# Kernel tuning notes

Hardware: AMD Instinct MI355X
Metric: run time of the kernel (lower is better)

## Reference

```python
import jax, jax.numpy as jnp
import numpy as np

N = 100000   # nodes
E = 1200000  # edges
NIN, EIN = 6, 1
HID, L, H = 64, 3, 4
D = HID // H  # 16 per-head dim


def setup_inputs() -> dict:
    key = jax.random.key(0)
    ks = jax.random.split(key, 20)
    r = lambda k, shape: (jax.random.normal(k, shape, dtype=jnp.float32) * 0.1)
    inp = {
        "x": jax.random.normal(ks[0], (N, NIN), dtype=jnp.float32),
        "edge_index": jax.random.randint(ks[1], (2, E), 0, N, dtype=jnp.int64),
        "edge_attr": jax.random.normal(ks[2], (E, EIN), dtype=jnp.float32),
        # node encoder (Linear-ReLU-Linear)
        "w_ne1": r(ks[3], (NIN, HID)), "b_ne1": jnp.zeros((HID,), jnp.float32),
        "w_ne2": r(ks[4], (HID, HID)), "b_ne2": jnp.zeros((HID,), jnp.float32),
        # edge encoder (Linear)
        "w_ee": r(ks[5], (EIN, HID)), "b_ee": jnp.zeros((HID,), jnp.float32),
        # stacked GAT layers (PyG GATConv w/ edge features, concat heads)
        "w_gat": r(ks[6], (L, HID, HID)),      # node lin per layer
        "w_eg": r(ks[7], (L, HID, HID)),       # edge lin per layer
        "att_src": r(ks[8], (L, H, D)),
        "att_dst": r(ks[9], (L, H, D)),
        "att_edge": r(ks[10], (L, H, D)),
        "b_gat": jnp.zeros((L, HID), jnp.float32),
        # per-layer LayerNorm
        "ln_g": jnp.ones((L, HID), jnp.float32),
        "ln_b": jnp.zeros((L, HID), jnp.float32),
        # output projection
        "w_out": r(ks[11], (HID, HID)), "b_out": jnp.zeros((HID,), jnp.float32),
    }
    return inp


def _layernorm(x, g, b, eps=1e-5):
    m = jnp.mean(x, axis=-1, keepdims=True)
    v = jnp.mean(jnp.square(x - m), axis=-1, keepdims=True)
    return (x - m) * jax.lax.rsqrt(v + eps) * g + b


def reference(x, edge_index, edge_attr, w_ne1, b_ne1, w_ne2, b_ne2, w_ee, b_ee,
              w_gat, w_eg, att_src, att_dst, att_edge, b_gat, ln_g, ln_b,
              w_out, b_out):
    n = x.shape[0]
    src, dst = edge_index[0], edge_index[1]
    # encode nodes / edges
    h = jax.nn.relu(x @ w_ne1 + b_ne1) @ w_ne2 + b_ne2          # [N, HID]
    e = edge_attr @ w_ee + b_ee                                  # [E, HID]
    num_layers = w_gat.shape[0]
    for l in range(num_layers):
        hw = (h @ w_gat[l]).reshape(n, H, D)                     # [N,H,D]
        ew = (e @ w_eg[l]).reshape(-1, H, D)                     # [E,H,D]
        a_s = jnp.sum(hw * att_src[l], axis=-1)                  # [N,H]
        a_d = jnp.sum(hw * att_dst[l], axis=-1)                  # [N,H]
        a_e = jnp.sum(ew * att_edge[l], axis=-1)                 # [E,H]
        score = jax.nn.leaky_relu(a_s[src] + a_d[dst] + a_e, 0.2)  # [E,H]
        # softmax over incoming edges of each destination node
        smax = jax.ops.segment_max(score, dst, num_segments=n)
        ex = jnp.exp(score - smax[dst])
        den = jax.ops.segment_sum(ex, dst, num_segments=n)
        alpha = ex / (den[dst] + 1e-16)                          # [E,H]
        msg = alpha[:, :, None] * hw[src]                        # [E,H,D]
        agg = jax.ops.segment_sum(msg, dst, num_segments=n)      # [N,H,D]
        agg = agg.reshape(n, H * D) + b_gat[l]
        h = _layernorm(h + jax.nn.elu(agg), ln_g[l], ln_b[l])
    return h @ w_out + b_out
```

## Files before the change

### kernel.cpp

```cpp
#include <hip/hip_runtime.h>

#define NIN 6
#define HIDN 64
#define NHEAD 4
#define DEGPAD 5

__device__ __forceinline__ unsigned short f2bf(float f) {
    unsigned u = __float_as_uint(f);
    unsigned r = (u >> 16) & 1u;
    return (unsigned short)((u + 0x7fffu + r) >> 16);
}

__device__ __forceinline__ void mm64_plain_body(
    const float* __restrict__ src, const float* __restrict__ W,
    const float* __restrict__ bias, float* __restrict__ dst, int N,
    int wv0, int nw) {
    int j = threadIdx.x & 63;
    float Wc[HIDN];
#pragma unroll
    for (int k = 0; k < HIDN; k++) Wc[k] = W[k * HIDN + j];
    float bj = bias[j];
    for (int n0 = wv0; n0 < N; n0 += nw) {
        int n = __builtin_amdgcn_readfirstlane(n0);
        const float4* __restrict__ row = (const float4*)(src + (size_t)n * HIDN);
        float a0 = 0.f, a1 = 0.f, a2 = 0.f, a3 = 0.f;
#pragma unroll
        for (int kk = 0; kk < 16; kk++) {
            float4 r = row[kk];
            a0 += r.x * Wc[4 * kk];
            a1 += r.y * Wc[4 * kk + 1];
            a2 += r.z * Wc[4 * kk + 2];
            a3 += r.w * Wc[4 * kk + 3];
        }
        dst[(size_t)n * HIDN + j] = ((a0 + a1) + (a2 + a3)) + bj;
    }
}

__device__ __forceinline__ void mm64_attn_body(
    const float* __restrict__ src, const float* __restrict__ W,
    const float* __restrict__ att_s, const float* __restrict__ att_d,
    unsigned short* __restrict__ dst16,
    float* __restrict__ a_s, float* __restrict__ a_d, int N,
    int wv0, int nw) {
    int j = threadIdx.x & 63;
    float Wc[HIDN];
#pragma unroll
    for (int k = 0; k < HIDN; k++) Wc[k] = W[k * HIDN + j];
    float asj = att_s[j];
    float adj = att_d[j];
    for (int n0 = wv0; n0 < N; n0 += nw) {
        int n = __builtin_amdgcn_readfirstlane(n0);
        const float4* __restrict__ row = (const float4*)(src + (size_t)n * HIDN);
        float a0 = 0.f, a1 = 0.f, a2 = 0.f, a3 = 0.f;
#pragma unroll
        for (int kk = 0; kk < 16; kk++) {
            float4 r = row[kk];
            a0 += r.x * Wc[4 * kk];
            a1 += r.y * Wc[4 * kk + 1];
            a2 += r.z * Wc[4 * kk + 2];
            a3 += r.w * Wc[4 * kk + 3];
        }
        float acc = (a0 + a1) + (a2 + a3);
        dst16[(size_t)n * HIDN + j] = f2bf(acc);
        float ts = acc * asj;
        float td = acc * adj;
#pragma unroll
        for (int o = 8; o > 0; o >>= 1) {
            ts += __shfl_xor(ts, o);
            td += __shfl_xor(td, o);
        }
        if ((j & 15) == 0) {
            a_s[(size_t)n * NHEAD + (j >> 4)] = ts;
            a_d[(size_t)n * NHEAD + (j >> 4)] = td;
        }
    }
}

__global__ __launch_bounds__(256) void pre_kernel(
    const int* __restrict__ ei, unsigned* __restrict__ deg,
    unsigned* __restrict__ rank, int E,
    const float* __restrict__ x, const float* __restrict__ w1,
    const float* __restrict__ b1, float* __restrict__ hid, int N,
    const float* __restrict__ w_ee, const float* __restrict__ b_ee,
    const float* __restrict__ w_eg, const float* __restrict__ att_edge,
    float* __restrict__ c1, float* __restrict__ c0,
    int histBlocks, int encBlocks) {
    int b = blockIdx.x;
    if (b < histBlocks) {
        int e = b * 256 + threadIdx.x;
        if (e < E) rank[e] = atomicAdd(&deg[(size_t)ei[E + e] << DEGPAD], 1u);
        return;
    }
    b -= histBlocks;
    if (b < encBlocks) {
        int t = b * 256 + threadIdx.x;
        int n = t >> 6, j = t & 63;
        if (n >= N) return;
        float acc = b1[j];
#pragma unroll
        for (int i = 0; i < NIN; i++) acc += x[n * NIN + i] * w1[i * HIDN + j];
        hid[(size_t)n * HIDN + j] = acc > 0.f ? acc : 0.f;
        return;
    }
    int w = threadIdx.x >> 6, j = threadIdx.x & 63;
    for (int p = w; p < 12; p += 4) {
        int l = p >> 2, hh = p & 3;
        const float* wr = w_eg + l * 4096 + j * 64 + hh * 16;
        const float* ae = att_edge + l * 64 + hh * 16;
        float wj = 0.f;
#pragma unroll
        for (int d = 0; d < 16; d++) wj += wr[d] * ae[d];
        float s1 = w_ee[j] * wj;
        float s0 = b_ee[j] * wj;
#pragma unroll
        for (int o = 32; o > 0; o >>= 1) {
            s1 += __shfl_xor(s1, o);
            s0 += __shfl_xor(s0, o);
        }
        if (j == 0) { c1[l * 4 + hh] = s1; c0[l * 4 + hh] = s0; }
    }
}

__global__ __launch_bounds__(256) void mid_kernel(
    const unsigned* __restrict__ deg, unsigned* __restrict__ rp,
    unsigned* __restrict__ bsum, int N,
    const float* __restrict__ src, const float* __restrict__ W,
    const float* __restrict__ bias, float* __restrict__ dst,
    int scanBlocks, int mmWaves) {
    __shared__ unsigned sm[256];
    int b = blockIdx.x;
    if (b < scanBlocks) {
        int t = threadIdx.x, i = b * 256 + t;
        unsigned v = (i < N) ? deg[(size_t)i << DEGPAD] : 0u;
        sm[t] = v;
        __syncthreads();
        unsigned xx = v;
        for (int o = 1; o < 256; o <<= 1) {
            unsigned add = (t >= o) ? sm[t - o] : 0u;
            __syncthreads();
            xx += add; sm[t] = xx;
            __syncthreads();
        }
        if (i < N) rp[i] = xx - v;
        if (t == 255) bsum[b] = xx;
        return;
    }
    int wv0 = ((b - scanBlocks) * 256 + threadIdx.x) >> 6;
    mm64_plain_body(src, W, bias, dst, N, wv0, mmWaves);
}

__global__ __launch_bounds__(256) void scan23_kernel(
    unsigned* __restrict__ rp, const unsigned* __restrict__ bsum,
    int N, int E) {
    __shared__ unsigned red[256];
    int b = blockIdx.x, t = threadIdx.x;
    unsigned partial = 0;
    for (int j = t; j < b; j += 256) partial += bsum[j];
    red[t] = partial;
    __syncthreads();
    for (int o = 128; o > 0; o >>= 1) {
        if (t < o) red[t] += red[t + o];
        __syncthreads();
    }
    unsigned off = red[0];
    int i = b * 256 + t;
    if (i < N) rp[i] += off;
    if (b == 0 && t == 0) rp[N] = (unsigned)E;
}

__global__ __launch_bounds__(256) void sca_kernel(
    const int* __restrict__ ei, const float* __restrict__ eattr,
    const unsigned* __restrict__ rp, const unsigned* __restrict__ rank,
    int2* __restrict__ eca, int E,
    const float* __restrict__ src, const float* __restrict__ W,
    const float* __restrict__ att_s, const float* __restrict__ att_d,
    unsigned short* __restrict__ dst16,
    float* __restrict__ a_s, float* __restrict__ a_d, int N,
    int scatBlocks, int mmWaves) {
    int b = blockIdx.x;
    if (b < scatBlocks) {
        int e = b * 256 + threadIdx.x;
        if (e >= E) return;
        int s = ei[e], d = ei[E + e];
        unsigned p = rp[d] + rank[e];
        eca[p] = make_int2(s, __float_as_int(eattr[e]));
        return;
    }
    int wv0 = ((b - scatBlocks) * 256 + threadIdx.x) >> 6;
    mm64_attn_body(src, W, att_s, att_d, dst16, a_s, a_d, N, wv0, mmWaves);
}

__global__ __launch_bounds__(256) void mm64_plain_kernel(
    const float* __restrict__ src, const float* __restrict__ W,
    const float* __restrict__ bias, float* __restrict__ dst, int N, int nw) {
    mm64_plain_body(src, W, bias, dst, N,
                    (blockIdx.x * blockDim.x + threadIdx.x) >> 6, nw);
}

__global__ __launch_bounds__(256) void mm64_attn_kernel(
    const float* __restrict__ src, const float* __restrict__ W,
    const float* __restrict__ att_s, const float* __restrict__ att_d,
    unsigned short* __restrict__ dst16,
    float* __restrict__ a_s, float* __restrict__ a_d, int N, int nw) {
    mm64_attn_body(src, W, att_s, att_d, dst16, a_s, a_d, N,
                   (blockIdx.x * blockDim.x + threadIdx.x) >> 6, nw);
}

__global__ __launch_bounds__(256) void gat_fused_kernel(
    const unsigned* __restrict__ rp, const int2* __restrict__ eca,
    const unsigned short* __restrict__ hw16,
    const float* __restrict__ a_s, const float* __restrict__ a_d,
    const float* __restrict__ c1, const float* __restrict__ c0,
    float* __restrict__ h, const float* __restrict__ bg,
    const float* __restrict__ g, const float* __restrict__ b, int N) {
    __shared__ float exl[4 * 272];
    __shared__ int srl[4 * 68];
    int t = blockIdx.x * blockDim.x + threadIdx.x;
    int lane = t & 63;
    int q = lane >> 4;
    int l = lane & 15;
    int hd = l >> 2;
    int sub = l & 3;
    int n = ((t >> 6) << 2) + q;
    int wslot = (threadIdx.x >> 6);
    float* myex = exl + wslot * 272 + 68 * q;
    int* mysrc = srl + wslot * 68 + 17 * q;

    bool nv = n < N;
    unsigned beg = nv ? rp[n] : 0u;
    int deg = nv ? (int)(rp[n + 1] - beg) : 0;

    float4 ad4 = nv ? *(const float4*)(a_d + ((size_t)n << 2)) : make_float4(0, 0, 0, 0);
    float4 C1 = *(const float4*)c1;
    float4 C0 = *(const float4*)c0;

    int md = deg;
    md = max(md, __shfl_xor(md, 16));
    md = max(md, __shfl_xor(md, 32));
    int chunks = (md + 15) >> 4;

    const unsigned* __restrict__ hwp = (const unsigned*)hw16;
    unsigned loff = (unsigned)(l << 1);

    float ssum = 0.f;
    float ac0 = 0.f, ac1 = 0.f, ac2 = 0.f, ac3 = 0.f;

    for (int k = 0; k < chunks; k++) {
        int i = (k << 4) + l;
        bool act = i < deg;
        int2 ce = act ? eca[beg + i] : make_int2(0, 0);
        int src = ce.x;
        float ea = __int_as_float(ce.y);
        float4 as4 = act ? *(const float4*)(a_s + ((size_t)src << 2))
                         : make_float4(0, 0, 0, 0);
        float s0 = as4.x + ad4.x + ea * C1.x + C0.x;
        float s1 = as4.y + ad4.y + ea * C1.y + C0.y;
        float s2 = as4.z + ad4.z + ea * C1.z + C0.z;
        float s3 = as4.w + ad4.w + ea * C1.w + C0.w;
        s0 = s0 >= 0.f ? s0 : 0.2f * s0;
        s1 = s1 >= 0.f ? s1 : 0.2f * s1;
        s2 = s2 >= 0.f ? s2 : 0.2f * s2;
        s3 = s3 >= 0.f ? s3 : 0.2f * s3;
        float e0 = act ? __expf(s0) : 0.f;
        float e1 = act ? __expf(s1) : 0.f;
        float e2 = act ? __expf(s2) : 0.f;
        float e3 = act ? __expf(s3) : 0.f;
        *(float4*)(myex + (l << 2)) = make_float4(e0, e1, e2, e3);
        mysrc[l] = act ? src : 0;

        float w0 = myex[(sub << 2) + hd];
        float w1 = myex[((sub + 4) << 2) + hd];
        float w2 = myex[((sub + 8) << 2) + hd];
        float w3 = myex[((sub + 12) << 2) + hd];
        float csum = (w0 + w1) + (w2 + w3);
        csum += __shfl_xor(csum, 1);
        csum += __shfl_xor(csum, 2);
        ssum += csum;

#pragma unroll
        for (int e = 0; e < 16; e++) {
            float w = myex[(e << 2) + hd];
            int so = mysrc[e];
            uint2 uu = *(const uint2*)(hwp + (((unsigned)so << 5) + loff));
            ac0 += w * __uint_as_float(uu.x << 16);
            ac1 += w * __uint_as_float(uu.x & 0xffff0000u);
            ac2 += w * __uint_as_float(uu.y << 16);
            ac3 += w * __uint_as_float(uu.y & 0xffff0000u);
        }
    }

    if (!nv) return;
    float inv = 1.f / (ssum + 1e-16f);
    float4 bg4 = *(const float4*)(bg + (l << 2));
    float4 hv4 = *(const float4*)(h + (size_t)n * HIDN + (l << 2));

    float a0 = ac0 * inv + bg4.x;
    float a1 = ac1 * inv + bg4.y;
    float a2 = ac2 * inv + bg4.z;
    float a3 = ac3 * inv + bg4.w;
    a0 = a0 > 0.f ? a0 : (__expf(a0) - 1.f);
    a1 = a1 > 0.f ? a1 : (__expf(a1) - 1.f);
    a2 = a2 > 0.f ? a2 : (__expf(a2) - 1.f);
    a3 = a3 > 0.f ? a3 : (__expf(a3) - 1.f);
    float v0 = hv4.x + a0, v1 = hv4.y + a1, v2 = hv4.z + a2, v3 = hv4.w + a3;

    float s = (v0 + v1) + (v2 + v3);
    float sq = (v0 * v0 + v1 * v1) + (v2 * v2 + v3 * v3);
#pragma unroll
    for (int o = 8; o > 0; o >>= 1) {
        s += __shfl_xor(s, o);
        sq += __shfl_xor(sq, o);
    }
    float mean = s * (1.f / 64.f);
    float var = sq * (1.f / 64.f) - mean * mean;
    float rr = rsqrtf(var + 1e-5f);
    float4 g4 = *(const float4*)(g + (l << 2));
    float4 b4 = *(const float4*)(b + (l << 2));
    float4 outv;
    outv.x = (v0 - mean) * rr * g4.x + b4.x;
    outv.y = (v1 - mean) * rr * g4.y + b4.y;
    outv.z = (v2 - mean) * rr * g4.z + b4.z;
    outv.w = (v3 - mean) * rr * g4.w + b4.w;
    *(float4*)(h + (size_t)n * HIDN + (l << 2)) = outv;
}

extern "C" void kernel_launch(void* const* d_in, const int* in_sizes, int n_in,
                              void* d_out, int out_size, void* d_ws, size_t ws_size,
                              hipStream_t stream) {
    const float* x      = (const float*)d_in[0];
    const int*   ei     = (const int*)d_in[1];
    const float* eattr  = (const float*)d_in[2];
    const float* w_ne1  = (const float*)d_in[3];
    const float* b_ne1  = (const float*)d_in[4];
    const float* w_ne2  = (const float*)d_in[5];
    const float* b_ne2  = (const float*)d_in[6];
    const float* w_ee   = (const float*)d_in[7];
    const float* b_ee   = (const float*)d_in[8];
    const float* w_gat  = (const float*)d_in[9];
    const float* w_eg   = (const float*)d_in[10];
    const float* att_src= (const float*)d_in[11];
    const float* att_dst= (const float*)d_in[12];
    const float* att_edge=(const float*)d_in[13];
    const float* b_gat  = (const float*)d_in[14];
    const float* ln_g   = (const float*)d_in[15];
    const float* ln_b   = (const float*)d_in[16];
    const float* w_out  = (const float*)d_in[17];
    const float* b_out  = (const float*)d_in[18];

    const int N = in_sizes[0] / NIN;
    const int E = in_sizes[2];

    float* ws   = (float*)d_ws;
    float* h    = ws;
    float* hid  = h + (size_t)N * 64;
    unsigned short* hw16 = (unsigned short*)(hid + (size_t)N * 64);
    float* a_s  = (float*)(hw16 + (size_t)N * 64);
    float* a_d  = a_s + (size_t)N * 4;
    float* c1   = a_d + (size_t)N * 4;
    float* c0   = c1 + 12;
    int2*  eca  = (int2*)(c0 + 12);
    unsigned* rank = (unsigned*)(eca + (size_t)E);
    unsigned* deg  = rank + (size_t)E;
    unsigned* rp   = deg + ((size_t)N << DEGPAD);
    unsigned* bsum = rp + (size_t)N + 1;
    unsigned* boff = bsum + 1024;
    (void)boff;

    dim3 blk(256);
    int edgeBlocks = (E + 255) / 256;
    int encBlocks  = (int)(((size_t)N * 64 + 255) / 256);
    int quadBlocks = (int)(((size_t)((N + 3) / 4) * 64 + 255) / 256);
    int nodeBlocks = (N + 255) / 256;
    int mmBlocks = 2048;
    int mmWaves  = mmBlocks * 4;

    hipMemsetAsync(deg, 0, ((size_t)N << DEGPAD) * sizeof(unsigned), stream);

    pre_kernel<<<edgeBlocks + encBlocks + 1, blk, 0, stream>>>(
        ei, deg, rank, E,
        x, w_ne1, b_ne1, hid, N,
        w_ee, b_ee, w_eg, att_edge, c1, c0,
        edgeBlocks, encBlocks);

    mid_kernel<<<nodeBlocks + mmBlocks, blk, 0, stream>>>(
        deg, rp, bsum, N, hid, w_ne2, b_ne2, h, nodeBlocks, mmWaves);

    scan23_kernel<<<nodeBlocks, blk, 0, stream>>>(rp, bsum, N, E);

    sca_kernel<<<edgeBlocks + mmBlocks, blk, 0, stream>>>(
        ei, eattr, rp, rank, eca, E,
        h, w_gat, att_src, att_dst, hw16, a_s, a_d, N,
        edgeBlocks, mmWaves);

    for (int l = 0; l < 3; l++) {
        gat_fused_kernel<<<quadBlocks, blk, 0, stream>>>(
            rp, eca, hw16, a_s, a_d, c1 + l * 4, c0 + l * 4,
            h, b_gat + l * 64, ln_g + l * 64, ln_b + l * 64, N);
        if (l < 2) {
            mm64_attn_kernel<<<mmBlocks, blk, 0, stream>>>(
                h, w_gat + (size_t)(l + 1) * 4096,
                att_src + (l + 1) * 64, att_dst + (l + 1) * 64,
                hw16, a_s, a_d, N, mmWaves);
        }
    }
    mm64_plain_kernel<<<mmBlocks, blk, 0, stream>>>(h, w_out, b_out, (float*)d_out, N, mmWaves);
}
```

Measured before the change: 464.4 us.

## Fuse full node encoder and first-layer GAT projection into pre kernel

The node encoder's first layer, second linear layer and the layer-0 GAT projection with attention logits are now computed in one wave-per-node loop inside the histogram/pre kernel, using cross-lane shuffles in place of memory round trips. This removes the intermediate hidden buffer and the separate matmul work in the mid and scatter kernels, which become plain scan and CSR-scatter kernels. The cost is heavy register use (two 64-float weight columns per lane) and 128 shuffles per node, which may limit occupancy of the fused kernel. It also shifts matmul work off the scan and scatter phases, so it no longer overlaps with them.

Measured after the change: 524.7 us. 13.0% more time.

```diff
diff --git a/kernel.cpp b/kernel.cpp
--- a/kernel.cpp
+++ b/kernel.cpp
@@ -80,11 +80,16 @@
     const int* __restrict__ ei, unsigned* __restrict__ deg,
     unsigned* __restrict__ rank, int E,
     const float* __restrict__ x, const float* __restrict__ w1,
-    const float* __restrict__ b1, float* __restrict__ hid, int N,
+    const float* __restrict__ b1,
+    const float* __restrict__ w2, const float* __restrict__ b2,
+    const float* __restrict__ wg, const float* __restrict__ att_s_w,
+    const float* __restrict__ att_d_w,
+    float* __restrict__ h, unsigned short* __restrict__ hw16,
+    float* __restrict__ a_s, float* __restrict__ a_d, int N,
     const float* __restrict__ w_ee, const float* __restrict__ b_ee,
     const float* __restrict__ w_eg, const float* __restrict__ att_edge,
     float* __restrict__ c1, float* __restrict__ c0,
-    int histBlocks, int encBlocks) {
+    int histBlocks, int encBlocks, int encWaves) {
     int b = blockIdx.x;
     if (b < histBlocks) {
         int e = b * 256 + threadIdx.x;
@@ -93,13 +98,59 @@
     }
     b -= histBlocks;
     if (b < encBlocks) {
-        int t = b * 256 + threadIdx.x;
-        int n = t >> 6, j = t & 63;
-        if (n >= N) return;
-        float acc = b1[j];
-#pragma unroll
-        for (int i = 0; i < NIN; i++) acc += x[n * NIN + i] * w1[i * HIDN + j];
-        hid[(size_t)n * HIDN + j] = acc > 0.f ? acc : 0.f;
+        int j = threadIdx.x & 63;
+        float Wa[NIN];
+#pragma unroll
+        for (int i = 0; i < NIN; i++) Wa[i] = w1[i * HIDN + j];
+        float b1j = b1[j];
+        float W2c[HIDN];
+#pragma unroll
+        for (int k = 0; k < HIDN; k++) W2c[k] = w2[k * HIDN + j];
+        float b2j = b2[j];
+        float Wgc[HIDN];
+#pragma unroll
+        for (int k = 0; k < HIDN; k++) Wgc[k] = wg[k * HIDN + j];
+        float asj = att_s_w[j];
+        float adj = att_d_w[j];
+        int wv0 = (b * 256 + (int)threadIdx.x) >> 6;
+        for (int n0 = wv0; n0 < N; n0 += encWaves) {
+            int n = __builtin_amdgcn_readfirstlane(n0);
+            float hv = b1j;
+#pragma unroll
+            for (int i = 0; i < NIN; i++) hv += x[(size_t)n * NIN + i] * Wa[i];
+            hv = hv > 0.f ? hv : 0.f;
+            float a0 = 0.f, a1 = 0.f, a2 = 0.f, a3 = 0.f;
+#pragma unroll
+            for (int kk = 0; kk < 16; kk++) {
+                a0 += __shfl(hv, 4 * kk)     * W2c[4 * kk];
+                a1 += __shfl(hv, 4 * kk + 1) * W2c[4 * kk + 1];
+                a2 += __shfl(hv, 4 * kk + 2) * W2c[4 * kk + 2];
+                a3 += __shfl(hv, 4 * kk + 3) * W2c[4 * kk + 3];
+            }
+            float hcur = ((a0 + a1) + (a2 + a3)) + b2j;
+            h[(size_t)n * HIDN + j] = hcur;
+            a0 = a1 = a2 = a3 = 0.f;
+#pragma unroll
+            for (int kk = 0; kk < 16; kk++) {
+                a0 += __shfl(hcur, 4 * kk)     * Wgc[4 * kk];
+                a1 += __shfl(hcur, 4 * kk + 1) * Wgc[4 * kk + 1];
+                a2 += __shfl(hcur, 4 * kk + 2) * Wgc[4 * kk + 2];
+                a3 += __shfl(hcur, 4 * kk + 3) * Wgc[4 * kk + 3];
+            }
+            float acc = (a0 + a1) + (a2 + a3);
+            hw16[(size_t)n * HIDN + j] = f2bf(acc);
+            float ts = acc * asj;
+            float td = acc * adj;
+#pragma unroll
+            for (int o = 8; o > 0; o >>= 1) {
+                ts += __shfl_xor(ts, o);
+                td += __shfl_xor(td, o);
+            }
+            if ((j & 15) == 0) {
+                a_s[(size_t)n * NHEAD + (j >> 4)] = ts;
+                a_d[(size_t)n * NHEAD + (j >> 4)] = td;
+            }
+        }
         return;
     }
     int w = threadIdx.x >> 6, j = threadIdx.x & 63;
@@ -121,32 +172,23 @@
     }
 }
 
-__global__ __launch_bounds__(256) void mid_kernel(
+__global__ __launch_bounds__(256) void scan1_kernel(
     const unsigned* __restrict__ deg, unsigned* __restrict__ rp,
-    unsigned* __restrict__ bsum, int N,
-    const float* __restrict__ src, const float* __restrict__ W,
-    const float* __restrict__ bias, float* __restrict__ dst,
-    int scanBlocks, int mmWaves) {
+    unsigned* __restrict__ bsum, int N) {
     __shared__ unsigned sm[256];
-    int b = blockIdx.x;
-    if (b < scanBlocks) {
-        int t = threadIdx.x, i = b * 256 + t;
-        unsigned v = (i < N) ? deg[(size_t)i << DEGPAD] : 0u;
-        sm[t] = v;
+    int t = threadIdx.x, i = blockIdx.x * 256 + t;
+    unsigned v = (i < N) ? deg[(size_t)i << DEGPAD] : 0u;
+    sm[t] = v;
+    __syncthreads();
+    unsigned xx = v;
+    for (int o = 1; o < 256; o <<= 1) {
+        unsigned add = (t >= o) ? sm[t - o] : 0u;
         __syncthreads();
-        unsigned xx = v;
-        for (int o = 1; o < 256; o <<= 1) {
-            unsigned add = (t >= o) ? sm[t - o] : 0u;
-            __syncthreads();
-            xx += add; sm[t] = xx;
-            __syncthreads();
-        }
-        if (i < N) rp[i] = xx - v;
-        if (t == 255) bsum[b] = xx;
-        return;
-    }
-    int wv0 = ((b - scanBlocks) * 256 + threadIdx.x) >> 6;
-    mm64_plain_body(src, W, bias, dst, N, wv0, mmWaves);
+        xx += add; sm[t] = xx;
+        __syncthreads();
+    }
+    if (i < N) rp[i] = xx - v;
+    if (t == 255) bsum[blockIdx.x] = xx;
 }
 
 __global__ __launch_bounds__(256) void scan23_kernel(
@@ -168,26 +210,15 @@
     if (b == 0 && t == 0) rp[N] = (unsigned)E;
 }
 
-__global__ __launch_bounds__(256) void sca_kernel(
+__global__ __launch_bounds__(256) void csr_scatter_kernel(
     const int* __restrict__ ei, const float* __restrict__ eattr,
     const unsigned* __restrict__ rp, const unsigned* __restrict__ rank,
-    int2* __restrict__ eca, int E,
-    const float* __restrict__ src, const float* __restrict__ W,
-    const float* __restrict__ att_s, const float* __restrict__ att_d,
-    unsigned short* __restrict__ dst16,
-    float* __restrict__ a_s, float* __restrict__ a_d, int N,
-    int scatBlocks, int mmWaves) {
-    int b = blockIdx.x;
-    if (b < scatBlocks) {
-        int e = b * 256 + threadIdx.x;
-        if (e >= E) return;
-        int s = ei[e], d = ei[E + e];
-        unsigned p = rp[d] + rank[e];
-        eca[p] = make_int2(s, __float_as_int(eattr[e]));
-        return;
-    }
-    int wv0 = ((b - scatBlocks) * 256 + threadIdx.x) >> 6;
-    mm64_attn_body(src, W, att_s, att_d, dst16, a_s, a_d, N, wv0, mmWaves);
+    int2* __restrict__ eca, int E) {
+    int e = blockIdx.x * 256 + threadIdx.x;
+    if (e >= E) return;
+    int s = ei[e], d = ei[E + e];
+    unsigned p = rp[d] + rank[e];
+    eca[p] = make_int2(s, __float_as_int(eattr[e]));
 }
 
 __global__ __launch_bounds__(256) void mm64_plain_kernel(
@@ -352,8 +383,7 @@
 
     float* ws   = (float*)d_ws;
     float* h    = ws;
-    float* hid  = h + (size_t)N * 64;
-    unsigned short* hw16 = (unsigned short*)(hid + (size_t)N * 64);
+    unsigned short* hw16 = (unsigned short*)(h + (size_t)N * 64);
     float* a_s  = (float*)(hw16 + (size_t)N * 64);
     float* a_d  = a_s + (size_t)N * 4;
     float* c1   = a_d + (size_t)N * 4;
@@ -363,34 +393,29 @@
     unsigned* deg  = rank + (size_t)E;
     unsigned* rp   = deg + ((size_t)N << DEGPAD);
     unsigned* bsum = rp + (size_t)N + 1;
-    unsigned* boff = bsum + 1024;
-    (void)boff;
 
     dim3 blk(256);
     int edgeBlocks = (E + 255) / 256;
-    int encBlocks  = (int)(((size_t)N * 64 + 255) / 256);
     int quadBlocks = (int)(((size_t)((N + 3) / 4) * 64 + 255) / 256);
     int nodeBlocks = (N + 255) / 256;
     int mmBlocks = 2048;
     int mmWaves  = mmBlocks * 4;
+    int encBlocks = 2048;
+    int encWaves  = encBlocks * 4;
 
     hipMemsetAsync(deg, 0, ((size_t)N << DEGPAD) * sizeof(unsigned), stream);
 
     pre_kernel<<<edgeBlocks + encBlocks + 1, blk, 0, stream>>>(
         ei, deg, rank, E,
-        x, w_ne1, b_ne1, hid, N,
+        x, w_ne1, b_ne1, w_ne2, b_ne2,
+        w_gat, att_src, att_dst,
+        h, hw16, a_s, a_d, N,
         w_ee, b_ee, w_eg, att_edge, c1, c0,
-        edgeBlocks, encBlocks);
-
-    mid_kernel<<<nodeBlocks + mmBlocks, blk, 0, stream>>>(
-        deg, rp, bsum, N, hid, w_ne2, b_ne2, h, nodeBlocks, mmWaves);
-
+        edgeBlocks, encBlocks, encWaves);
+
+    scan1_kernel<<<nodeBlocks, blk, 0, stream>>>(deg, rp, bsum, N);
     scan23_kernel<<<nodeBlocks, blk, 0, stream>>>(rp, bsum, N, E);
-
-    sca_kernel<<<edgeBlocks + mmBlocks, blk, 0, stream>>>(
-        ei, eattr, rp, rank, eca, E,
-        h, w_gat, att_src, att_dst, hw16, a_s, a_d, N,
-        edgeBlocks, mmWaves);
+    csr_scatter_kernel<<<edgeBlocks, blk, 0, stream>>>(ei, eattr, rp, rank, eca, E);
 
     for (int l = 0; l < 3; l++) {
         gat_fused_kernel<<<quadBlocks, blk, 0, stream>>>(
```

## Fuse next-layer projection and output matmul into GAT aggregation kernel

Applied to the files above, without the earlier changes.

Each GAT layer kernel now loads the next layer's 64x64 weight into shared memory and, after LayerNorm, computes the next hw projection, bf16 pack, and attention logits in place. The last layer computes the output linear directly. This removes three separate mm64 launches and the re-read of h from global memory. Ping-pong buffers reuse the hid region so the current layer's hw16 is never overwritten while it is still being read. The cost is 16KB of extra LDS per block, which may lower occupancy for the latency-bound gather, plus a 4096-float weight load in every block.

Result: faster. 429.6 us (median of 2 runs) (-7.5%).

```diff
diff --git a/kernel.cpp b/kernel.cpp
--- a/kernel.cpp
+++ b/kernel.cpp
@@ -190,31 +190,31 @@
     mm64_attn_body(src, W, att_s, att_d, dst16, a_s, a_d, N, wv0, mmWaves);
 }
 
-__global__ __launch_bounds__(256) void mm64_plain_kernel(
-    const float* __restrict__ src, const float* __restrict__ W,
-    const float* __restrict__ bias, float* __restrict__ dst, int N, int nw) {
-    mm64_plain_body(src, W, bias, dst, N,
-                    (blockIdx.x * blockDim.x + threadIdx.x) >> 6, nw);
-}
-
-__global__ __launch_bounds__(256) void mm64_attn_kernel(
-    const float* __restrict__ src, const float* __restrict__ W,
-    const float* __restrict__ att_s, const float* __restrict__ att_d,
-    unsigned short* __restrict__ dst16,
-    float* __restrict__ a_s, float* __restrict__ a_d, int N, int nw) {
-    mm64_attn_body(src, W, att_s, att_d, dst16, a_s, a_d, N,
-                   (blockIdx.x * blockDim.x + threadIdx.x) >> 6, nw);
-}
-
-__global__ __launch_bounds__(256) void gat_fused_kernel(
+template <int MODE>
+__global__ __launch_bounds__(256) void gat_fused_x_kernel(
     const unsigned* __restrict__ rp, const int2* __restrict__ eca,
     const unsigned short* __restrict__ hw16,
     const float* __restrict__ a_s, const float* __restrict__ a_d,
     const float* __restrict__ c1, const float* __restrict__ c0,
     float* __restrict__ h, const float* __restrict__ bg,
-    const float* __restrict__ g, const float* __restrict__ b, int N) {
+    const float* __restrict__ g, const float* __restrict__ b, int N,
+    const float* __restrict__ Wnext,
+    const float* __restrict__ att_s_w, const float* __restrict__ att_d_w,
+    const float* __restrict__ bias_out,
+    unsigned short* __restrict__ hw16_out,
+    float* __restrict__ a_s_out, float* __restrict__ a_d_out,
+    float* __restrict__ out) {
+    __shared__ float WgL[4096];
     __shared__ float exl[4 * 272];
     __shared__ int srl[4 * 68];
+
+    {
+        const float4* __restrict__ Wn4 = (const float4*)Wnext;
+        float4* WgL4 = (float4*)WgL;
+        for (int i = threadIdx.x; i < 1024; i += 256) WgL4[i] = Wn4[i];
+    }
+    __syncthreads();
+
     int t = blockIdx.x * blockDim.x + threadIdx.x;
     int lane = t & 63;
     int q = lane >> 4;
@@ -289,10 +289,10 @@
         }
     }
 
-    if (!nv) return;
     float inv = 1.f / (ssum + 1e-16f);
     float4 bg4 = *(const float4*)(bg + (l << 2));
-    float4 hv4 = *(const float4*)(h + (size_t)n * HIDN + (l << 2));
+    float4 hv4 = nv ? *(const float4*)(h + (size_t)n * HIDN + (l << 2))
+                    : make_float4(0, 0, 0, 0);
 
     float a0 = ac0 * inv + bg4.x;
     float a1 = ac1 * inv + bg4.y;
@@ -316,12 +316,60 @@
     float rr = rsqrtf(var + 1e-5f);
     float4 g4 = *(const float4*)(g + (l << 2));
     float4 b4 = *(const float4*)(b + (l << 2));
-    float4 outv;
-    outv.x = (v0 - mean) * rr * g4.x + b4.x;
-    outv.y = (v1 - mean) * rr * g4.y + b4.y;
-    outv.z = (v2 - mean) * rr * g4.z + b4.z;
-    outv.w = (v3 - mean) * rr * g4.w + b4.w;
-    *(float4*)(h + (size_t)n * HIDN + (l << 2)) = outv;
+    v0 = (v0 - mean) * rr * g4.x + b4.x;
+    v1 = (v1 - mean) * rr * g4.y + b4.y;
+    v2 = (v2 - mean) * rr * g4.z + b4.z;
+    v3 = (v3 - mean) * rr * g4.w + b4.w;
+
+    if (MODE == 0 && nv) {
+        *(float4*)(h + (size_t)n * HIDN + (l << 2)) = make_float4(v0, v1, v2, v3);
+    }
+
+    float* stg = exl + wslot * 272;
+    *(float4*)(stg + (q << 6) + (l << 2)) = make_float4(v0, v1, v2, v3);
+
+    float4 A0 = make_float4(0, 0, 0, 0), A1 = make_float4(0, 0, 0, 0);
+    float4 A2 = make_float4(0, 0, 0, 0), A3 = make_float4(0, 0, 0, 0);
+#pragma unroll
+    for (int kk = 0; kk < 16; kk++) {
+        float4 hk = *(const float4*)(stg + (q << 6) + (kk << 2));
+        const float* wr = WgL + (kk << 8) + (l << 2);
+        float4 w0 = *(const float4*)(wr);
+        float4 w1 = *(const float4*)(wr + 64);
+        float4 w2 = *(const float4*)(wr + 128);
+        float4 w3 = *(const float4*)(wr + 192);
+        A0.x += hk.x * w0.x; A0.y += hk.x * w0.y; A0.z += hk.x * w0.z; A0.w += hk.x * w0.w;
+        A1.x += hk.y * w1.x; A1.y += hk.y * w1.y; A1.z += hk.y * w1.z; A1.w += hk.y * w1.w;
+        A2.x += hk.z * w2.x; A2.y += hk.z * w2.y; A2.z += hk.z * w2.z; A2.w += hk.z * w2.w;
+        A3.x += hk.w * w3.x; A3.y += hk.w * w3.y; A3.z += hk.w * w3.z; A3.w += hk.w * w3.w;
+    }
+    float o0 = (A0.x + A1.x) + (A2.x + A3.x);
+    float o1 = (A0.y + A1.y) + (A2.y + A3.y);
+    float o2 = (A0.z + A1.z) + (A2.z + A3.z);
+    float o3 = (A0.w + A1.w) + (A2.w + A3.w);
+
+    if (MODE == 0) {
+        if (nv) {
+            ushort4 pk = make_ushort4(f2bf(o0), f2bf(o1), f2bf(o2), f2bf(o3));
+            *(ushort4*)(hw16_out + (size_t)n * HIDN + (l << 2)) = pk;
+        }
+        float4 asw = *(const float4*)(att_s_w + (l << 2));
+        float4 adw = *(const float4*)(att_d_w + (l << 2));
+        float ts = (o0 * asw.x + o1 * asw.y) + (o2 * asw.z + o3 * asw.w);
+        float td = (o0 * adw.x + o1 * adw.y) + (o2 * adw.z + o3 * adw.w);
+        ts += __shfl_xor(ts, 1); ts += __shfl_xor(ts, 2);
+        td += __shfl_xor(td, 1); td += __shfl_xor(td, 2);
+        if (nv && (l & 3) == 0) {
+            a_s_out[(size_t)n * NHEAD + (l >> 2)] = ts;
+            a_d_out[(size_t)n * NHEAD + (l >> 2)] = td;
+        }
+    } else {
+        if (nv) {
+            float4 bo = *(const float4*)(bias_out + (l << 2));
+            *(float4*)(out + (size_t)n * HIDN + (l << 2)) =
+                make_float4(o0 + bo.x, o1 + bo.y, o2 + bo.z, o3 + bo.w);
+        }
+    }
 }
 
 extern "C" void kernel_launch(void* const* d_in, const int* in_sizes, int n_in,
@@ -363,8 +411,10 @@
     unsigned* deg  = rank + (size_t)E;
     unsigned* rp   = deg + ((size_t)N << DEGPAD);
     unsigned* bsum = rp + (size_t)N + 1;
-    unsigned* boff = bsum + 1024;
-    (void)boff;
+
+    unsigned short* hw16b = (unsigned short*)hid;
+    float* a_sb = (float*)(hw16b + (size_t)N * 64);
+    float* a_db = a_sb + (size_t)N * 4;
 
     dim3 blk(256);
     int edgeBlocks = (E + 255) / 256;
@@ -392,16 +442,21 @@
         h, w_gat, att_src, att_dst, hw16, a_s, a_d, N,
         edgeBlocks, mmWaves);
 
-    for (int l = 0; l < 3; l++) {
-        gat_fused_kernel<<<quadBlocks, blk, 0, stream>>>(
-            rp, eca, hw16, a_s, a_d, c1 + l * 4, c0 + l * 4,
-            h, b_gat + l * 64, ln_g + l * 64, ln_b + l * 64, N);
-        if (l < 2) {
-            mm64_attn_kernel<<<mmBlocks, blk, 0, stream>>>(
-                h, w_gat + (size_t)(l + 1) * 4096,
-                att_src + (l + 1) * 64, att_dst + (l + 1) * 64,
-                hw16, a_s, a_d, N, mmWaves);
-        }
-    }
-    mm64_plain_kernel<<<mmBlocks, blk, 0, stream>>>(h, w_out, b_out, (float*)d_out, N, mmWaves);
-}
+    gat_fused_x_kernel<0><<<quadBlocks, blk, 0, stream>>>(
+        rp, eca, hw16, a_s, a_d, c1 + 0, c0 + 0,
+        h, b_gat + 0, ln_g + 0, ln_b + 0, N,
+        w_gat + (size_t)1 * 4096, att_src + 64, att_dst + 64, nullptr,
+        hw16b, a_sb, a_db, nullptr);
+
+    gat_fused_x_kernel<0><<<quadBlocks, blk, 0, stream>>>(
+        rp, eca, hw16b, a_sb, a_db, c1 + 4, c0 + 4,
+        h, b_gat + 64, ln_g + 64, ln_b + 64, N,
+        w_gat + (size_t)2 * 4096, att_src + 2 * 64, att_dst + 2 * 64, nullptr,
+        hw16, a_s, a_d, nullptr);
+
+    gat_fused_x_kernel<1><<<quadBlocks, blk, 0, stream>>>(
+        rp, eca, hw16, a_s, a_d, c1 + 8, c0 + 8,
+        h, b_gat + 2 * 64, ln_g + 2 * 64, ln_b + 2 * 64, N,
+        w_out, nullptr, nullptr, b_out,
+        nullptr, nullptr, nullptr, (float*)d_out);
+}
```
